# Kernel optimization log

Hardware: AMD Instinct MI355X
Metric: run time of the kernel (lower is better)

## Reference

```python
import jax, jax.numpy as jnp
import numpy as np

B, S, F, E, H, L = 16, 256, 512, 128, 64, 8


def _gru(x, Wih, Whh, bih, bhh):
    """torch-style GRU over time. x: [B,S,E] -> hidden states [B,S,H]."""
    xp = jnp.einsum('bse,ge->bsg', x, Wih) + bih  # [B,S,3H]

    def step(h, xt):
        gh = h @ Whh.T + bhh                      # [B,3H]
        xr, xz, xn = jnp.split(xt, 3, axis=-1)
        hr, hz, hn = jnp.split(gh, 3, axis=-1)
        r = jax.nn.sigmoid(xr + hr)
        z = jax.nn.sigmoid(xz + hz)
        n = jnp.tanh(xn + r * hn)
        h_new = (1.0 - z) * n + z * h
        return h_new, h_new

    h0 = jnp.zeros((x.shape[0], Whh.shape[1]), x.dtype)
    _, hs = jax.lax.scan(step, h0, jnp.swapaxes(xp, 0, 1))  # [S,B,H]
    return jnp.swapaxes(hs, 0, 1)


def setup_inputs() -> dict:
    ks = jax.random.split(jax.random.key(0), 24)
    u = lambda k, shape, n: jax.random.uniform(k, shape, jnp.float32, -1.0 / np.sqrt(n), 1.0 / np.sqrt(n))
    inp = {
        'X': jax.random.normal(ks[0], (B, S, F), jnp.float32),
        'M': jnp.ones((B, S), jnp.float32),
        'cur_M': jax.random.uniform(ks[1], (B, S), jnp.float32),
        # embed linear [E,F]
        'W_embed': u(ks[2], (E, F), F), 'b_embed': u(ks[3], (E,), F),
        # GRU alpha
        'Wih_a': u(ks[4], (3 * H, E), H), 'Whh_a': u(ks[5], (3 * H, H), H),
        'bih_a': u(ks[6], (3 * H,), H), 'bhh_a': u(ks[7], (3 * H,), H),
        # GRU beta
        'Wih_b': u(ks[8], (3 * H, E), H), 'Whh_b': u(ks[9], (3 * H, H), H),
        'bih_b': u(ks[10], (3 * H,), H), 'bhh_b': u(ks[11], (3 * H,), H),
        # attention linears
        'Wb': u(ks[12], (E, H), H), 'bb': u(ks[13], (E,), H),
        'Wa': u(ks[14], (1, H), H), 'ba': u(ks[15], (1,), H),
        # predict linear
        'Wp': u(ks[16], (L, E), E), 'bp': u(ks[17], (L,), E),
    }
    return inp


def reference(X, M, cur_M, W_embed, b_embed,
              Wih_a, Whh_a, bih_a, bhh_a,
              Wih_b, Whh_b, bih_b, bhh_b,
              Wb, bb, Wa, ba, Wp, bp):
    n_seq = X.shape[1]
    emb = jnp.einsum('bsf,ef->bse', X, W_embed) + b_embed          # [B,S,E]
    h_alpha = _gru(emb, Wih_a, Whh_a, bih_a, bhh_a)                # [B,S,H]
    h_beta = _gru(emb, Wih_b, Whh_b, bih_b, bhh_b)                 # [B,S,H]

    # RETAIN attention
    beta_w = jnp.tanh(jnp.einsum('bsh,eh->bse', h_beta, Wb) + bb)  # [B,S,E]
    corr = (jnp.einsum('bsh,oh->bso', h_alpha, Wa) + ba)[..., 0]   # [B,S]
    attn = jnp.exp(corr)                                           # [B,S] (indexed by j)
    flag = jnp.triu(jnp.ones((n_seq, n_seq), X.dtype))             # flag[i,j]=1 iff j>=i
    flag_m = flag[None, :, :] * M[:, None, :]                      # [B,S,S]
    num = attn[:, None, :] * flag_m                                # [B,i,j]
    denom = num.sum(-1, keepdims=True) + 1e-10                     # [B,S,1]
    alpha_w = num / denom                                          # [B,S,S]
    # sum_j alpha[b,i,j] * beta_w[b,j,:] * emb[b,j,:]  (same math as the
    # original broadcasted [B,S,S,E] product, without materializing it)
    weighted = jnp.einsum('bij,bje->bie', alpha_w, beta_w * emb)   # [B,S,E]

    all_output = (jnp.einsum('bse,le->bsl', weighted, Wp) + bp) * M[..., None]  # [B,S,L]
    cur_output = (all_output * cur_M[..., None]).sum(axis=1)                    # [B,L]
    return all_output, cur_output
```

## Files before the change

kernel.cpp:

```cpp
#include <hip/hip_runtime.h>
#include <math.h>

#define BB 16
#define SS 256
#define FF 512
#define EE 128
#define HH 64
#define GG 192
#define LL 8
#define TT 16

__device__ __forceinline__ float sigmoid_f(float x) {
    return 1.0f / (1.0f + __expf(-x));
}
__device__ __forceinline__ float tanh_f(float x) {
    return 1.0f - 2.0f / (1.0f + __expf(2.0f * x));
}

__device__ __forceinline__ void gemm_bt_body(
    const float* __restrict__ A, const float* __restrict__ Bm,
    const float* __restrict__ bias, float* __restrict__ C,
    int N, int K)
{
    __shared__ float As[32][68];
    __shared__ float Bs[64][68];
    const int t = threadIdx.x;
    const int row0 = blockIdx.x * 32;
    const int col0 = blockIdx.y * 64;
    const int tr = t & 7;
    const int tc = t >> 3;
    float acc[4][2] = {{0.f,0.f},{0.f,0.f},{0.f,0.f},{0.f,0.f}};

    for (int k0 = 0; k0 < K; k0 += 64) {
        {
            int r = t >> 3;
            int q = t & 7;
            const float* src = &A[(size_t)(row0 + r) * K + k0];
            #pragma unroll
            for (int it = 0; it < 2; ++it) {
                int kk = (q + it * 8) * 4;
                *(float4*)&As[r][kk] = *(const float4*)&src[kk];
            }
        }
        {
            int r = t >> 2;
            int q = t & 3;
            int n = col0 + r;
            #pragma unroll
            for (int it = 0; it < 4; ++it) {
                int kk = (q + it * 4) * 4;
                float4 v = {0.f, 0.f, 0.f, 0.f};
                if (n < N) v = *(const float4*)&Bm[(size_t)n * K + k0 + kk];
                *(float4*)&Bs[r][kk] = v;
            }
        }
        __syncthreads();
        #pragma unroll
        for (int k = 0; k < 64; k += 4) {
            float4 av[4], bv[2];
            #pragma unroll
            for (int i = 0; i < 4; ++i) av[i] = *(const float4*)&As[tr + 8*i][k];
            #pragma unroll
            for (int j = 0; j < 2; ++j) bv[j] = *(const float4*)&Bs[tc + 32*j][k];
            #pragma unroll
            for (int i = 0; i < 4; ++i)
                #pragma unroll
                for (int j = 0; j < 2; ++j)
                    acc[i][j] += av[i].x*bv[j].x + av[i].y*bv[j].y
                               + av[i].z*bv[j].z + av[i].w*bv[j].w;
        }
        __syncthreads();
    }

    #pragma unroll
    for (int i = 0; i < 4; ++i) {
        int r = row0 + tr + 8*i;
        #pragma unroll
        for (int j = 0; j < 2; ++j) {
            int c = col0 + tc + 32*j;
            if (c < N) C[(size_t)r * N + c] = acc[i][j] + bias[c];
        }
    }
}

__global__ __launch_bounds__(256) void gemm_bt(
    const float* __restrict__ A, const float* __restrict__ Bm,
    const float* __restrict__ bias, float* __restrict__ C,
    int N, int K)
{
    gemm_bt_body(A, Bm, bias, C, N, K);
}

__global__ __launch_bounds__(256) void gemm_bt_dual(
    const float* __restrict__ A,
    const float* __restrict__ B0, const float* __restrict__ bias0, float* __restrict__ C0,
    const float* __restrict__ B1, const float* __restrict__ bias1, float* __restrict__ C1,
    int N, int K)
{
    const float* Bm   = blockIdx.z ? B1    : B0;
    const float* bias = blockIdx.z ? bias1 : bias0;
    float*       C    = blockIdx.z ? C1    : C0;
    gemm_bt_body(A, Bm, bias, C, N, K);
}

__global__ __launch_bounds__(192, 1)
__attribute__((amdgpu_waves_per_eu(1, 1)))
void gru_kernel(
    const float* __restrict__ xpa, const float* __restrict__ xpb,
    const float* __restrict__ Whh_a, const float* __restrict__ bhh_a,
    const float* __restrict__ Whh_b, const float* __restrict__ bhh_b,
    float* __restrict__ hs_a, float* __restrict__ hs_b)
{
    const int blk = blockIdx.x;
    const int b = blk >> 1;
    const int which = blk & 1;
    const float* xp  = which ? xpb   : xpa;
    const float* Whh = which ? Whh_b : Whh_a;
    const float* bhh = which ? bhh_b : bhh_a;
    float* hs        = which ? hs_b  : hs_a;

    const int t = threadIdx.x;
    const int g = t >> 6;
    const int j = t & 63;

    __shared__ float gh_s[2][GG];

    const float4* wrow = (const float4*)&Whh[(size_t)(g * 64 + j) * HH];
    float4 w0  = wrow[0],  w1  = wrow[1],  w2  = wrow[2],  w3  = wrow[3];
    float4 w4  = wrow[4],  w5  = wrow[5],  w6  = wrow[6],  w7  = wrow[7];
    float4 w8  = wrow[8],  w9  = wrow[9],  w10 = wrow[10], w11 = wrow[11];
    float4 w12 = wrow[12], w13 = wrow[13], w14 = wrow[14], w15 = wrow[15];

    const float bh = bhh[g * 64 + j];

    const float* xrow = xp + (size_t)b * SS * GG;
    float* hrow = hs + (size_t)b * SS * HH;
    float hcur = 0.f;

    float xg = xrow[g * 64 + j];
    float xn = xrow[128 + j];

#define RL(v, k) __int_as_float(__builtin_amdgcn_readlane(__float_as_int(v), (k)))
#define DOT4(W, i)                                  \
    a0 = fmaf(W.x, RL(hcur, 4*(i) + 0), a0);        \
    a1 = fmaf(W.y, RL(hcur, 4*(i) + 1), a1);        \
    a2 = fmaf(W.z, RL(hcur, 4*(i) + 2), a2);        \
    a3 = fmaf(W.w, RL(hcur, 4*(i) + 3), a3);

    for (int s = 0; s < SS; ++s) {
        const float* nx = xrow + GG;
        float nxg = nx[g * 64 + j];
        float nxn = nx[128 + j];

        float a0 = bh, a1 = 0.f, a2 = 0.f, a3 = 0.f;
        DOT4(w0, 0)   DOT4(w1, 1)   DOT4(w2, 2)   DOT4(w3, 3)
        DOT4(w4, 4)   DOT4(w5, 5)   DOT4(w6, 6)   DOT4(w7, 7)
        DOT4(w8, 8)   DOT4(w9, 9)   DOT4(w10, 10) DOT4(w11, 11)
        DOT4(w12, 12) DOT4(w13, 13) DOT4(w14, 14) DOT4(w15, 15)
        float pre = (a0 + a1) + (a2 + a3);
        gh_s[s & 1][t] = (g < 2) ? (xg + pre) : pre;

        asm volatile("s_waitcnt lgkmcnt(0)" ::: "memory");
        __builtin_amdgcn_s_barrier();
        asm volatile("" ::: "memory");

        float ghr = gh_s[s & 1][j];
        float ghz = gh_s[s & 1][64 + j];
        float ghn = gh_s[s & 1][128 + j];
        float r = sigmoid_f(ghr);
        float z = sigmoid_f(ghz);
        float n = tanh_f(xn + r * ghn);
        hcur = fmaf(z, hcur - n, n);
        if (g == 0) hrow[j] = hcur;

        xg = nxg; xn = nxn;
        xrow += GG;
        hrow += HH;
    }
#undef DOT4
#undef RL
}

__global__ __launch_bounds__(128) void attn_val_kernel(
    const float* __restrict__ h_alpha, const float* __restrict__ h_beta,
    const float* __restrict__ emb, const float* __restrict__ M,
    const float* __restrict__ Wa, const float* __restrict__ ba,
    const float* __restrict__ Wb, const float* __restrict__ bb,
    float* __restrict__ val, float* __restrict__ wj)
{
    const int bj = blockIdx.x;
    const int t = threadIdx.x;
    __shared__ float hb_s[HH];
    __shared__ float wj_s;

    if (t < 64) {
        hb_s[t] = h_beta[(size_t)bj * HH + t];
        float p = h_alpha[(size_t)bj * HH + t] * Wa[t];
        #pragma unroll
        for (int off = 32; off > 0; off >>= 1) p += __shfl_down(p, off);
        if (t == 0) {
            float a = __expf(p + ba[0]) * M[bj];
            wj_s = a;
            wj[bj] = a;
        }
    }
    __syncthreads();

    float acc = bb[t];
    const float4* wrow = (const float4*)&Wb[(size_t)t * HH];
    #pragma unroll
    for (int k = 0; k < 16; ++k) {
        float4 w4 = wrow[k];
        float4 h4 = *(const float4*)&hb_s[k * 4];
        acc += w4.x*h4.x + w4.y*h4.y + w4.z*h4.z + w4.w*h4.w;
    }
    float bw = tanh_f(acc);
    val[(size_t)bj * EE + t] = bw * emb[(size_t)bj * EE + t] * wj_s;
}

__global__ __launch_bounds__(128) void scanA_kernel(
    const float* __restrict__ val, const float* __restrict__ wj,
    float* __restrict__ tsum, float* __restrict__ wsum)
{
    const int b = blockIdx.x, tt = blockIdx.y;
    const int e = threadIdx.x;
    const int j0 = tt * 16;
    float s = 0.f;
    #pragma unroll
    for (int jj = 0; jj < 16; ++jj)
        s += val[((size_t)(b * SS + j0 + jj)) * EE + e];
    tsum[((size_t)(b * TT + tt)) * EE + e] = s;

    if (e < 16) {
        float p = wj[b * SS + j0 + e];
        #pragma unroll
        for (int off = 8; off > 0; off >>= 1) p += __shfl_down(p, off, 16);
        if (e == 0) wsum[b * TT + tt] = p;
    }
}

__global__ __launch_bounds__(128) void scanB_kernel(
    const float* __restrict__ val, const float* __restrict__ wj,
    const float* __restrict__ tsum, const float* __restrict__ wsum,
    float* __restrict__ wtd)
{
    const int b = blockIdx.x, tt = blockIdx.y;
    const int e = threadIdx.x;
    const int j0 = tt * 16;

    float se = 0.f;
    for (int t2 = tt + 1; t2 < TT; ++t2)
        se += tsum[((size_t)(b * TT + t2)) * EE + e];
    float d = 1e-10f;
    for (int t2 = tt + 1; t2 < TT; ++t2)
        d += wsum[b * TT + t2];

    for (int jj = 15; jj >= 0; --jj) {
        size_t idx = ((size_t)(b * SS + j0 + jj)) * EE + e;
        se += val[idx];
        d += wj[b * SS + j0 + jj];
        wtd[idx] = se / d;
    }
}

__global__ __launch_bounds__(256) void proj_kernel(
    const float* __restrict__ wtd, const float* __restrict__ Wp,
    const float* __restrict__ bp, const float* __restrict__ M,
    float* __restrict__ out)
{
    __shared__ float wt_s[32][132];
    __shared__ float wp_s[8][132];
    const int t = threadIdx.x;
    const int row0 = blockIdx.x * 32;

    {
        int r = t >> 3;
        int q = t & 7;
        const float* src = &wtd[(size_t)(row0 + r) * EE];
        #pragma unroll
        for (int it = 0; it < 4; ++it) {
            int kk = (q + it * 8) * 4;
            *(float4*)&wt_s[r][kk] = *(const float4*)&src[kk];
        }
    }
    {
        int r = t >> 5;
        int q = t & 31;
        *(float4*)&wp_s[r][q * 4] = *(const float4*)&Wp[(size_t)r * EE + q * 4];
    }
    __syncthreads();

    const int r = t >> 3, l = t & 7;
    float acc = 0.f;
    #pragma unroll
    for (int i = 0; i < 32; ++i) {
        float4 a = *(const float4*)&wt_s[r][i * 4];
        float4 w = *(const float4*)&wp_s[l][i * 4];
        acc += a.x*w.x + a.y*w.y + a.z*w.z + a.w*w.w;
    }
    const int row = row0 + r;
    out[(size_t)row * LL + l] = (acc + bp[l]) * M[row];
}

__global__ __launch_bounds__(256) void cur_kernel(
    const float* __restrict__ out_all, const float* __restrict__ curM,
    float* __restrict__ out_cur)
{
    const int b = blockIdx.x;
    const int t = threadIdx.x;
    const int l = t & 7, c = t >> 3;
    float p = 0.f;
    #pragma unroll
    for (int k = 0; k < 8; ++k) {
        int s = c + k * 32;
        p += out_all[((size_t)(b * SS + s)) * LL + l] * curM[b * SS + s];
    }
    __shared__ float red[32][9];
    red[c][l] = p;
    __syncthreads();
    if (t < 8) {
        float sum = 0.f;
        for (int c2 = 0; c2 < 32; ++c2) sum += red[c2][t];
        out_cur[b * LL + t] = sum;
    }
}

extern "C" void kernel_launch(void* const* d_in, const int* in_sizes, int n_in,
                              void* d_out, int out_size, void* d_ws, size_t ws_size,
                              hipStream_t stream)
{
    const float* X       = (const float*)d_in[0];
    const float* M       = (const float*)d_in[1];
    const float* cur_M   = (const float*)d_in[2];
    const float* W_embed = (const float*)d_in[3];
    const float* b_embed = (const float*)d_in[4];
    const float* Wih_a   = (const float*)d_in[5];
    const float* Whh_a   = (const float*)d_in[6];
    const float* bih_a   = (const float*)d_in[7];
    const float* bhh_a   = (const float*)d_in[8];
    const float* Wih_b   = (const float*)d_in[9];
    const float* Whh_b   = (const float*)d_in[10];
    const float* bih_b   = (const float*)d_in[11];
    const float* bhh_b   = (const float*)d_in[12];
    const float* Wb      = (const float*)d_in[13];
    const float* bb      = (const float*)d_in[14];
    const float* Wa      = (const float*)d_in[15];
    const float* ba      = (const float*)d_in[16];
    const float* Wp      = (const float*)d_in[17];
    const float* bp      = (const float*)d_in[18];
    float* out = (float*)d_out;

    float* ws  = (float*)d_ws;
    float* emb = ws;
    float* xpa = emb + (size_t)BB*SS*EE;
    float* xpb = xpa + (size_t)BB*SS*GG;
    float* ha  = xpb + (size_t)BB*SS*GG;
    float* hb  = ha  + (size_t)BB*SS*HH;
    float* val = hb  + (size_t)BB*SS*HH;
    float* wjv = val + (size_t)BB*SS*EE;
    float* wtd = wjv + (size_t)BB*SS;
    float* tsum = wtd + (size_t)BB*SS*EE;
    float* wsum = tsum + (size_t)BB*TT*EE;

    const int ROWS = BB * SS;

    gemm_bt<<<dim3(ROWS/32, EE/64), 256, 0, stream>>>(X, W_embed, b_embed, emb, EE, FF);
    gemm_bt_dual<<<dim3(ROWS/32, (GG+63)/64, 2), 256, 0, stream>>>(
        emb, Wih_a, bih_a, xpa, Wih_b, bih_b, xpb, GG, EE);
    gru_kernel<<<32, 192, 0, stream>>>(xpa, xpb, Whh_a, bhh_a, Whh_b, bhh_b, ha, hb);
    attn_val_kernel<<<ROWS, 128, 0, stream>>>(ha, hb, emb, M, Wa, ba, Wb, bb, val, wjv);
    scanA_kernel<<<dim3(BB, TT), 128, 0, stream>>>(val, wjv, tsum, wsum);
    scanB_kernel<<<dim3(BB, TT), 128, 0, stream>>>(val, wjv, tsum, wsum, wtd);
    proj_kernel<<<ROWS/32, 256, 0, stream>>>(wtd, Wp, bp, M, out);
    cur_kernel<<<BB, 256, 0, stream>>>(out, cur_M, out + (size_t)BB*SS*LL);
}
```

Measured before the change: 175.1 us.

## Fuse attention with block-sum scan and suffix scan with output projection

Merges the per-row attention-value kernel with the per-tile sum kernel, so each block walks its 16 rows and accumulates tile sums in registers. The suffix-scan kernel now keeps the normalized weighted rows in shared memory and applies the Wp projection directly. This drops two launches and the global write and read of the intermediate weighted tensor. In exchange the attention stage runs on only 256 blocks, processing rows serially with two barriers per row, which lowers parallelism for that phase.

Result: no change. 173.1 us (median of 2 runs) (-1.2%).

```diff
diff --git a/kernel.cpp b/kernel.cpp
--- a/kernel.cpp
+++ b/kernel.cpp
@@ -181,112 +181,92 @@
 #undef RL
 }
 
-__global__ __launch_bounds__(128) void attn_val_kernel(
+__global__ __launch_bounds__(128) void attn_scanA_kernel(
     const float* __restrict__ h_alpha, const float* __restrict__ h_beta,
     const float* __restrict__ emb, const float* __restrict__ M,
     const float* __restrict__ Wa, const float* __restrict__ ba,
     const float* __restrict__ Wb, const float* __restrict__ bb,
-    float* __restrict__ val, float* __restrict__ wj)
-{
-    const int bj = blockIdx.x;
-    const int t = threadIdx.x;
+    float* __restrict__ val, float* __restrict__ wj,
+    float* __restrict__ tsum, float* __restrict__ wsum)
+{
+    const int b = blockIdx.x, tt = blockIdx.y;
+    const int t = threadIdx.x;
+    const int j0 = tt * 16;
     __shared__ float hb_s[HH];
     __shared__ float wj_s;
 
-    if (t < 64) {
-        hb_s[t] = h_beta[(size_t)bj * HH + t];
-        float p = h_alpha[(size_t)bj * HH + t] * Wa[t];
+    const float bbt = bb[t];
+    const float4* wrow = (const float4*)&Wb[(size_t)t * HH];
+
+    float ts = 0.f;
+    float ws = 0.f;
+
+    for (int jj = 0; jj < 16; ++jj) {
+        const int row = b * SS + j0 + jj;
+        if (t < 64) {
+            hb_s[t] = h_beta[(size_t)row * HH + t];
+            float p = h_alpha[(size_t)row * HH + t] * Wa[t];
+            #pragma unroll
+            for (int off = 32; off > 0; off >>= 1) p += __shfl_down(p, off);
+            if (t == 0) {
+                float a = __expf(p + ba[0]) * M[row];
+                wj_s = a;
+                wj[row] = a;
+            }
+        }
+        __syncthreads();
+
+        float acc = bbt;
         #pragma unroll
-        for (int off = 32; off > 0; off >>= 1) p += __shfl_down(p, off);
-        if (t == 0) {
-            float a = __expf(p + ba[0]) * M[bj];
-            wj_s = a;
-            wj[bj] = a;
-        }
-    }
-    __syncthreads();
-
-    float acc = bb[t];
-    const float4* wrow = (const float4*)&Wb[(size_t)t * HH];
-    #pragma unroll
-    for (int k = 0; k < 16; ++k) {
-        float4 w4 = wrow[k];
-        float4 h4 = *(const float4*)&hb_s[k * 4];
-        acc += w4.x*h4.x + w4.y*h4.y + w4.z*h4.z + w4.w*h4.w;
-    }
-    float bw = tanh_f(acc);
-    val[(size_t)bj * EE + t] = bw * emb[(size_t)bj * EE + t] * wj_s;
-}
-
-__global__ __launch_bounds__(128) void scanA_kernel(
-    const float* __restrict__ val, const float* __restrict__ wj,
-    float* __restrict__ tsum, float* __restrict__ wsum)
-{
-    const int b = blockIdx.x, tt = blockIdx.y;
-    const int e = threadIdx.x;
-    const int j0 = tt * 16;
-    float s = 0.f;
-    #pragma unroll
-    for (int jj = 0; jj < 16; ++jj)
-        s += val[((size_t)(b * SS + j0 + jj)) * EE + e];
-    tsum[((size_t)(b * TT + tt)) * EE + e] = s;
-
-    if (e < 16) {
-        float p = wj[b * SS + j0 + e];
-        #pragma unroll
-        for (int off = 8; off > 0; off >>= 1) p += __shfl_down(p, off, 16);
-        if (e == 0) wsum[b * TT + tt] = p;
-    }
-}
-
-__global__ __launch_bounds__(128) void scanB_kernel(
+        for (int k = 0; k < 16; ++k) {
+            float4 w4 = wrow[k];
+            float4 h4 = *(const float4*)&hb_s[k * 4];
+            acc += w4.x*h4.x + w4.y*h4.y + w4.z*h4.z + w4.w*h4.w;
+        }
+        float v = tanh_f(acc) * emb[(size_t)row * EE + t] * wj_s;
+        val[(size_t)row * EE + t] = v;
+        ts += v;
+        if (t == 0) ws += wj_s;
+        __syncthreads();
+    }
+
+    tsum[((size_t)(b * TT + tt)) * EE + t] = ts;
+    if (t == 0) wsum[b * TT + tt] = ws;
+}
+
+__global__ __launch_bounds__(128) void scanB_proj_kernel(
     const float* __restrict__ val, const float* __restrict__ wj,
     const float* __restrict__ tsum, const float* __restrict__ wsum,
-    float* __restrict__ wtd)
+    const float* __restrict__ Wp, const float* __restrict__ bp,
+    const float* __restrict__ M, float* __restrict__ out)
 {
     const int b = blockIdx.x, tt = blockIdx.y;
-    const int e = threadIdx.x;
+    const int t = threadIdx.x;
     const int j0 = tt * 16;
+
+    __shared__ float wtd_s[16][132];
+    __shared__ float wp_s[8][132];
 
     float se = 0.f;
     for (int t2 = tt + 1; t2 < TT; ++t2)
-        se += tsum[((size_t)(b * TT + t2)) * EE + e];
+        se += tsum[((size_t)(b * TT + t2)) * EE + t];
     float d = 1e-10f;
     for (int t2 = tt + 1; t2 < TT; ++t2)
         d += wsum[b * TT + t2];
 
     for (int jj = 15; jj >= 0; --jj) {
-        size_t idx = ((size_t)(b * SS + j0 + jj)) * EE + e;
+        size_t idx = ((size_t)(b * SS + j0 + jj)) * EE + t;
         se += val[idx];
         d += wj[b * SS + j0 + jj];
-        wtd[idx] = se / d;
-    }
-}
-
-__global__ __launch_bounds__(256) void proj_kernel(
-    const float* __restrict__ wtd, const float* __restrict__ Wp,
-    const float* __restrict__ bp, const float* __restrict__ M,
-    float* __restrict__ out)
-{
-    __shared__ float wt_s[32][132];
-    __shared__ float wp_s[8][132];
-    const int t = threadIdx.x;
-    const int row0 = blockIdx.x * 32;
-
-    {
-        int r = t >> 3;
-        int q = t & 7;
-        const float* src = &wtd[(size_t)(row0 + r) * EE];
-        #pragma unroll
-        for (int it = 0; it < 4; ++it) {
-            int kk = (q + it * 8) * 4;
-            *(float4*)&wt_s[r][kk] = *(const float4*)&src[kk];
-        }
-    }
-    {
-        int r = t >> 5;
-        int q = t & 31;
-        *(float4*)&wp_s[r][q * 4] = *(const float4*)&Wp[(size_t)r * EE + q * 4];
+        wtd_s[jj][t] = se / d;
+    }
+
+    #pragma unroll
+    for (int it = 0; it < 2; ++it) {
+        int idx = t + it * 128;
+        int r = idx >> 5;
+        int c = idx & 31;
+        *(float4*)&wp_s[r][c * 4] = *(const float4*)&Wp[(size_t)r * EE + c * 4];
     }
     __syncthreads();
 
@@ -294,11 +274,11 @@
     float acc = 0.f;
     #pragma unroll
     for (int i = 0; i < 32; ++i) {
-        float4 a = *(const float4*)&wt_s[r][i * 4];
+        float4 a = *(const float4*)&wtd_s[r][i * 4];
         float4 w = *(const float4*)&wp_s[l][i * 4];
         acc += a.x*w.x + a.y*w.y + a.z*w.z + a.w*w.w;
     }
-    const int row = row0 + r;
+    const int row = b * SS + j0 + r;
     out[(size_t)row * LL + l] = (acc + bp[l]) * M[row];
 }
 
@@ -358,8 +338,7 @@
     float* hb  = ha  + (size_t)BB*SS*HH;
     float* val = hb  + (size_t)BB*SS*HH;
     float* wjv = val + (size_t)BB*SS*EE;
-    float* wtd = wjv + (size_t)BB*SS;
-    float* tsum = wtd + (size_t)BB*SS*EE;
+    float* tsum = wjv + (size_t)BB*SS;
     float* wsum = tsum + (size_t)BB*TT*EE;
 
     const int ROWS = BB * SS;
@@ -368,9 +347,9 @@
     gemm_bt_dual<<<dim3(ROWS/32, (GG+63)/64, 2), 256, 0, stream>>>(
         emb, Wih_a, bih_a, xpa, Wih_b, bih_b, xpb, GG, EE);
     gru_kernel<<<32, 192, 0, stream>>>(xpa, xpb, Whh_a, bhh_a, Whh_b, bhh_b, ha, hb);
-    attn_val_kernel<<<ROWS, 128, 0, stream>>>(ha, hb, emb, M, Wa, ba, Wb, bb, val, wjv);
-    scanA_kernel<<<dim3(BB, TT), 128, 0, stream>>>(val, wjv, tsum, wsum);
-    scanB_kernel<<<dim3(BB, TT), 128, 0, stream>>>(val, wjv, tsum, wsum, wtd);
-    proj_kernel<<<ROWS/32, 256, 0, stream>>>(wtd, Wp, bp, M, out);
+    attn_scanA_kernel<<<dim3(BB, TT), 128, 0, stream>>>(
+        ha, hb, emb, M, Wa, ba, Wb, bb, val, wjv, tsum, wsum);
+    scanB_proj_kernel<<<dim3(BB, TT), 128, 0, stream>>>(
+        val, wjv, tsum, wsum, Wp, bp, M, out);
     cur_kernel<<<BB, 256, 0, stream>>>(out, cur_M, out + (size_t)BB*SS*LL);
 }
```
